# Kernel tuning notes

Hardware: AMD Instinct MI355X
Metric: run time of the kernel (lower is better)

Reference implementation:

```python
import jax, jax.numpy as jnp
import numpy as np

NEG_INF = jnp.float32(-1e30)


def setup_inputs() -> dict:
    key = jax.random.key(0)
    k1, k2, k3, k4 = jax.random.split(key, 4)
    B, L1, L2, H = 64, 1024, 1024, 128
    x = jax.random.normal(k1, (B, L1, H), dtype=jnp.float32)
    y = jax.random.normal(k2, (B, L2, H), dtype=jnp.float32)
    y_mask = jax.random.uniform(k3, (B, L2)) < 0.2
    W = jax.random.normal(k4, (H, H), dtype=jnp.float32) * (1.0 / np.sqrt(H))
    b = jnp.zeros((H,), dtype=jnp.float32)
    return {"x": x, "y": y, "y_mask": y_mask, "W": W, "b": b}


def reference(x, y, y_mask, W, b):
    # shared linear + relu projections (torch Linear: x @ W.T + b)
    x_proj = jax.nn.relu(jnp.einsum("bld,hd->blh", x, W) + b)  # [B, L1, H]
    y_proj = jax.nn.relu(jnp.einsum("bld,hd->blh", y, W) + b)  # [B, L2, H]
    # unscaled cross-attention scores
    scores = jnp.einsum("bih,bjh->bij", x_proj, y_proj)  # [B, L1, L2]
    scores = jnp.where(y_mask[:, None, :], NEG_INF, scores)
    alpha = jax.nn.softmax(scores, axis=-1)  # [B, L1, L2]
    # weighted sum over original (unprojected) y
    matched_seq = jnp.einsum("bij,bjh->bih", alpha, y)  # [B, L1, H]
    return matched_seq
```

## Files before the change

kernel.cpp:

```cpp
#include <hip/hip_runtime.h>
#include <hip/hip_bf16.h>


typedef __attribute__((ext_vector_type(8))) short    s8v;
typedef __attribute__((ext_vector_type(8))) _Float16 h8v;
typedef __attribute__((ext_vector_type(4))) float    f4v;

#define BDIM 256

__device__ __forceinline__ f4v mfma_bf16(s8v a, s8v b, f4v c) {
    return __builtin_amdgcn_mfma_f32_16x16x32_bf16(a, b, c, 0, 0, 0);
}
__device__ __forceinline__ f4v mfma_f16(h8v a, h8v b, f4v c) {
    return __builtin_amdgcn_mfma_f32_16x16x32_f16(a, b, c, 0, 0, 0);
}
__device__ __forceinline__ void tsplit(float v, short& hi, short& lo) {
    unsigned b = __builtin_bit_cast(unsigned, v);
    unsigned hb = b & 0xFFFF0000u;
    float res = v - __builtin_bit_cast(float, hb);
    hi = (short)(hb >> 16);
    lo = (short)(__builtin_bit_cast(unsigned, res) >> 16);
}

typedef const __attribute__((address_space(1))) unsigned int gu32;
typedef __attribute__((address_space(3))) unsigned int lu32;
__device__ __forceinline__ void gld_lds16(const void* g, void* l) {
    __builtin_amdgcn_global_load_lds((gu32*)g, (lu32*)l, 16, 0, 0);
}

__global__ __launch_bounds__(1024) void prep_kernel(
    const unsigned int* __restrict__ mraw, unsigned char* __restrict__ nm,
    const float* __restrict__ W, short* __restrict__ Whsw, short* __restrict__ Wlsw,
    const float* __restrict__ Y, _Float16* __restrict__ YTsw)
{
    if (blockIdx.x >= 2) {
        const int tb = blockIdx.x - 2;
        const int b = tb >> 4, jt = tb & 15;
        __shared__ _Float16 sT[128][64];
        const int tid = threadIdx.x;
        const int h = tid & 127, c0 = tid >> 7;
        const float* yb = Y + (size_t)(b * 1024 + jt * 64 + c0 * 8) * 128 + h;
        h8v hv;
        for (int k = 0; k < 8; ++k) hv[k] = (_Float16)yb[k * 128];
        *(h8v*)&sT[h][(c0 ^ (h & 7)) << 3] = hv;
        __syncthreads();
        *(h8v*)(YTsw + (size_t)tb * 8192 + tid * 8) =
            *(const h8v*)(&sT[0][0] + tid * 8);
        return;
    }
    if (blockIdx.x == 1) {
        for (int idx = threadIdx.x; idx < 16384; idx += 1024) {
            int r = idx >> 7, c = idx & 127;
            short hi, lo; tsplit(W[idx], hi, lo);
            int cs = (((c >> 3) ^ (r & 15)) << 3) | (c & 7);
            Whsw[r * 128 + cs] = hi;
            Wlsw[r * 128 + cs] = lo;
        }
        return;
    }
    __shared__ unsigned int sOrAll, sOrOdd;
    if (threadIdx.x == 0) { sOrAll = 0u; sOrOdd = 0u; }
    __syncthreads();
    unsigned int oa = 0u, oo = 0u;
    for (int i = threadIdx.x; i < 16384; i += 1024) {
        unsigned int v = mraw[i];
        oa |= v;
        if (i & 1) oo |= v;
    }
    atomicOr(&sOrAll, oa);
    atomicOr(&sOrOdd, oo);
    __syncthreads();
    const unsigned int orv = sOrAll, oro = sOrOdd;
    int mode;
    if (orv <= 1u)                       mode = (orv == 1u && oro == 0u) ? 3 : 0;
    else if ((orv & 0xFEFEFEFEu) == 0u)  mode = 1;
    else if ((orv & 0x0000FFFFu) == 0u)  mode = 0;
    else                                 mode = 2;
    const unsigned char*  b8  = (const unsigned char*)mraw;
    const unsigned short* b16 = (const unsigned short*)mraw;
    for (int j = threadIdx.x; j < 65536; j += 1024) {
        unsigned int v;
        if (mode == 0)      v = mraw[j];
        else if (mode == 1) v = b8[j];
        else if (mode == 2) v = b16[j];
        else                v = mraw[2 * j] | mraw[2 * j + 1];
        nm[j] = v ? 1 : 0;
    }
}

__global__ __launch_bounds__(BDIM, 4) void proj_kernel(
    const float* __restrict__ X, const float* __restrict__ Y,
    const short* __restrict__ Whsw, const short* __restrict__ Wlsw,
    const float* __restrict__ bias,
    _Float16* __restrict__ XPf, _Float16* __restrict__ YPsw)
{
    __shared__ short sW[2][64][128];

    const int gid = blockIdx.x;
    const float* src; int local;
    if (gid < 1024) { src = X; local = gid; }
    else            { src = Y; local = gid - 1024; }
    const int row0 = (local >> 1) * 128, h0 = (local & 1) * 64;
    const int t = threadIdx.x, w = t >> 6, lane = t & 63, c = lane & 15, q = lane >> 4;

    {
        const short* g0 = Whsw + h0 * 128;
        const short* g1 = Wlsw + h0 * 128;
        short* l0 = &sW[0][0][0];
        short* l1 = &sW[1][0][0];
        for (int i = 0; i < 4; ++i) {
            int off = (t + i * BDIM) * 8;
            *(s8v*)(l0 + off) = *(const s8v*)(g0 + off);
            *(s8v*)(l1 + off) = *(const s8v*)(g1 + off);
        }
    }

    f4v rawA[2][4], rawB[2][4];
#pragma unroll
    for (int set = 0; set < 2; ++set) {
        const float* xr = src + (size_t)(row0 + w * 32 + set * 16 + c) * 128;
#pragma unroll
        for (int ks = 0; ks < 4; ++ks) {
            rawA[set][ks] = *(const f4v*)&xr[ks * 32 + q * 8];
            rawB[set][ks] = *(const f4v*)&xr[ks * 32 + q * 8 + 4];
        }
    }
    __syncthreads();

    f4v zero = {0.f, 0.f, 0.f, 0.f};
#pragma unroll
    for (int set = 0; set < 2; ++set) {
        s8v ah[4], al[4];
#pragma unroll
        for (int ks = 0; ks < 4; ++ks) {
            for (int k = 0; k < 4; ++k) {
                short hh, ll;
                tsplit(rawA[set][ks][k], hh, ll); ah[ks][k] = hh;     al[ks][k] = ll;
                tsplit(rawB[set][ks][k], hh, ll); ah[ks][4 + k] = hh; al[ks][4 + k] = ll;
            }
        }
        f4v acc[4];
        for (int n = 0; n < 4; ++n) acc[n] = zero;
#pragma unroll
        for (int ks = 0; ks < 4; ++ks) {
            s8v bh[4], bl[4];
            for (int nt = 0; nt < 4; ++nt) {
                int cs = (((ks * 4 + q) ^ c) << 3);
                bh[nt] = *(const s8v*)&sW[0][nt * 16 + c][cs];
                bl[nt] = *(const s8v*)&sW[1][nt * 16 + c][cs];
            }
            for (int nt = 0; nt < 4; ++nt) {
                acc[nt] = mfma_bf16(ah[ks], bh[nt], acc[nt]);
                acc[nt] = mfma_bf16(al[ks], bh[nt], acc[nt]);
                acc[nt] = mfma_bf16(ah[ks], bl[nt], acc[nt]);
            }
        }
        for (int nt = 0; nt < 4; ++nt) {
            float bv = bias[h0 + nt * 16 + c];
            for (int r = 0; r < 4; ++r) {
                float v = fmaxf(acc[nt][r] + bv, 0.0f);
                int grow = row0 + w * 32 + set * 16 + q * 4 + r;
                int h = h0 + nt * 16 + c;
                if (gid < 1024) {
                    XPf[(size_t)grow * 128 + h] = (_Float16)v;
                } else {
                    int jt = (grow >> 6) & 15, jr = grow & 63;
                    int chunk = (h >> 3) ^ (jr & 7);
                    size_t off = (size_t)((grow >> 10) * 16 + jt) * 8192
                                 + jr * 128 + chunk * 8 + (h & 7);
                    YPsw[off] = (_Float16)v;
                }
            }
        }
    }
}

__global__ __launch_bounds__(BDIM, 2) void attn_kernel(
    const _Float16* __restrict__ YPsw, const _Float16* __restrict__ YTsw,
    const unsigned char* __restrict__ nmask,
    const _Float16* __restrict__ XPf, float* __restrict__ out)
{
    __shared__ _Float16 sTile[2][16384];
    __shared__ _Float16 sP[64][72];

    const int id = blockIdx.x;
    const int xcd = id & 7, rest = id >> 3;
    const int ibase = (rest & 15) * 64;
    const int b = xcd + 8 * (rest >> 4);
    const int t = threadIdx.x, wave = t >> 6, lane = t & 63;
    const int c = lane & 15, q = lane >> 4;
    const int mrow = b * 1024;

    h8v afrag[4];
    {
        const _Float16* xr = XPf + (size_t)(mrow + ibase + wave * 16 + c) * 128;
        for (int ks = 0; ks < 4; ++ks)
            afrag[ks] = *(const h8v*)&xr[ks * 32 + q * 8];
    }

    const char* gYP = (const char*)(YPsw + (size_t)b * 16 * 8192);
    const char* gYT = (const char*)(YTsw + (size_t)b * 16 * 8192);
    const int soff = wave * 1024 + lane * 16;

    {
        const char* gp = gYP + soff;
        const char* gt = gYT + soff;
        char* lp = (char*)&sTile[0][0]    + wave * 1024;
        char* lt = (char*)&sTile[0][8192] + wave * 1024;
        for (int i = 0; i < 4; ++i) {
            gld_lds16(gp + i * 4096, lp + i * 4096);
            gld_lds16(gt + i * 4096, lt + i * 4096);
        }
    }

    unsigned mw[4];
    for (int nt = 0; nt < 4; ++nt)
        mw[nt] = *(const unsigned*)(nmask + mrow + nt * 16 + q * 4);

    f4v zero = {0.f, 0.f, 0.f, 0.f};
    float m_s = -INFINITY, l_s = 0.f;
    f4v o[8];
    for (int h = 0; h < 8; ++h) o[h] = zero;

    const int srcbase = (lane & 48) + ((lane >> 4) << 2);
    const int cb = q ^ (c & 7);

    __syncthreads();

    int cur = 0;
    for (int jt = 0; jt < 16; ++jt) {
        const int jbase = jt * 64;
        const int nx = cur ^ 1;

        if (jt < 15) {
            const char* gp = gYP + (size_t)(jt + 1) * 16384 + soff;
            const char* gt = gYT + (size_t)(jt + 1) * 16384 + soff;
            char* lp = (char*)&sTile[nx][0]    + wave * 1024;
            char* lt = (char*)&sTile[nx][8192] + wave * 1024;
            for (int i = 0; i < 4; ++i) {
                gld_lds16(gp + i * 4096, lp + i * 4096);
                gld_lds16(gt + i * 4096, lt + i * 4096);
            }
        }

        f4v s[4];
        __builtin_amdgcn_s_setprio(1);
        for (int nt = 0; nt < 4; ++nt) {
            const _Float16* rp = &sTile[cur][0] + (nt * 16 + c) * 128;
            h8v f0 = *(const h8v*)(rp + ((cb ^ 0) << 3));
            h8v f1 = *(const h8v*)(rp + ((cb ^ 4) << 3));
            h8v f2 = *(const h8v*)(rp + ((cb ^ 8) << 3));
            h8v f3 = *(const h8v*)(rp + ((cb ^ 12) << 3));
            f4v acc = zero;
            acc = mfma_f16(f0, afrag[0], acc);
            acc = mfma_f16(f1, afrag[1], acc);
            acc = mfma_f16(f2, afrag[2], acc);
            acc = mfma_f16(f3, afrag[3], acc);
            s[nt] = acc;
        }
        __builtin_amdgcn_s_setprio(0);

        for (int nt = 0; nt < 4; ++nt)
            for (int r = 0; r < 4; ++r)
                if ((mw[nt] >> (r * 8)) & 0xFFu) s[nt][r] = -1e30f;

        float mx = fmaxf(
            fmaxf(fmaxf(fmaxf(s[0][0], s[0][1]), fmaxf(s[0][2], s[0][3])),
                  fmaxf(fmaxf(s[1][0], s[1][1]), fmaxf(s[1][2], s[1][3]))),
            fmaxf(fmaxf(fmaxf(s[2][0], s[2][1]), fmaxf(s[2][2], s[2][3])),
                  fmaxf(fmaxf(s[3][0], s[3][1]), fmaxf(s[3][2], s[3][3]))));
        mx = fmaxf(mx, __shfl_xor(mx, 16, 64));
        mx = fmaxf(mx, __shfl_xor(mx, 32, 64));
        float mnew = fmaxf(m_s, mx);
        float alpha = __expf(m_s - mnew);
        m_s = mnew;

        float rsum = 0.f;
        for (int nt = 0; nt < 4; ++nt)
            for (int r = 0; r < 4; ++r) {
                float p = ((mw[nt] >> (r * 8)) & 0xFFu) ? 0.f
                          : __expf(s[nt][r] - mnew);
                _Float16 ph = (_Float16)p;
                rsum += (float)ph;
                sP[wave * 16 + c][nt * 16 + q * 4 + r] = ph;
            }
        rsum += __shfl_xor(rsum, 16, 64);
        rsum += __shfl_xor(rsum, 32, 64);
        l_s = l_s * alpha + rsum;

        if (jt < 15) {
            const int jn = jbase + 64;
            for (int nt = 0; nt < 4; ++nt)
                mw[nt] = *(const unsigned*)(nmask + mrow + jn + nt * 16 + q * 4);
        }

        float aD0 = __shfl(alpha, srcbase + 0, 64);
        float aD1 = __shfl(alpha, srcbase + 1, 64);
        float aD2 = __shfl(alpha, srcbase + 2, 64);
        float aD3 = __shfl(alpha, srcbase + 3, 64);
        for (int h = 0; h < 8; ++h) {
            o[h][0] *= aD0; o[h][1] *= aD1; o[h][2] *= aD2; o[h][3] *= aD3;
        }

        __builtin_amdgcn_s_setprio(1);
        for (int k2 = 0; k2 < 2; ++k2) {
            h8v a = *(const h8v*)&sP[wave * 16 + c][k2 * 32 + q * 8];
            const _Float16* yt = &sTile[cur][8192];
            for (int hb = 0; hb < 8; ++hb) {
                h8v bb = *(const h8v*)(yt + (hb * 16 + c) * 64
                                       + ((((k2 << 2) + q) ^ (c & 7)) << 3));
                o[hb] = mfma_f16(a, bb, o[hb]);
            }
        }
        __builtin_amdgcn_s_setprio(0);

        __syncthreads();
        cur = nx;
    }

    float lD[4];
    lD[0] = __shfl(l_s, srcbase + 0, 64);
    lD[1] = __shfl(l_s, srcbase + 1, 64);
    lD[2] = __shfl(l_s, srcbase + 2, 64);
    lD[3] = __shfl(l_s, srcbase + 3, 64);
    for (int h = 0; h < 8; ++h) {
        for (int r = 0; r < 4; ++r) {
            float v = o[h][r] / lD[r];
            out[(size_t)(mrow + ibase + wave * 16 + q * 4 + r) * 128 + h * 16 + c] = v;
        }
    }
}

extern "C" void kernel_launch(void* const* d_in, const int* in_sizes, int n_in,
                              void* d_out, int out_size, void* d_ws, size_t ws_size,
                              hipStream_t stream) {
    const float* x    = (const float*)d_in[0];
    const float* y    = (const float*)d_in[1];
    const unsigned int* mraw = (const unsigned int*)d_in[2];
    const float* W    = (const float*)d_in[3];
    const float* bias = (const float*)d_in[4];
    float* out = (float*)d_out;

    unsigned char* nmask = (unsigned char*)d_ws;
    short* Whsw = (short*)((char*)d_ws + 65536);
    short* Wlsw = Whsw + 16384;
    _Float16* XPf = (_Float16*)(Wlsw + 16384);
    _Float16* YPsw = XPf + (size_t)64 * 1024 * 128;
    _Float16* YTsw = YPsw + (size_t)64 * 1024 * 128;

    prep_kernel<<<1026, 1024, 0, stream>>>(mraw, nmask, W, Whsw, Wlsw, y, YTsw);
    proj_kernel<<<2048, BDIM, 0, stream>>>(x, y, Whsw, Wlsw, bias, XPf, YPsw);
    attn_kernel<<<1024, BDIM, 0, stream>>>(YPsw, YTsw, nmask, XPf, out);
}
```

Measured before the change: 227.7 us.

## Double attention block to 128 query rows and swizzle P tile in LDS

Each attention block now handles 128 query rows with 8 waves (512 threads) instead of 64 rows with 4 waves. The shared Y tiles are therefore reused by twice as many rows, which halves the global-to-LDS traffic per query row, and each thread issues half as many async loads. The P staging buffer is rewritten with XOR-swizzled 4-wide vector stores, replacing scalar padded stores, to reduce LDS bank conflicts and store count. The trade-off is fewer blocks in the grid (512), which may lower occupancy and latency hiding, plus more LDS use per block.

```diff
diff --git a/kernel.cpp b/kernel.cpp
--- a/kernel.cpp
+++ b/kernel.cpp
@@ -4,6 +4,7 @@
 
 typedef __attribute__((ext_vector_type(8))) short    s8v;
 typedef __attribute__((ext_vector_type(8))) _Float16 h8v;
+typedef __attribute__((ext_vector_type(4))) _Float16 h4v;
 typedef __attribute__((ext_vector_type(4))) float    f4v;
 
 #define BDIM 256
@@ -175,18 +176,18 @@
     }
 }
 
-__global__ __launch_bounds__(BDIM, 2) void attn_kernel(
+__global__ __launch_bounds__(512, 4) void attn_kernel(
     const _Float16* __restrict__ YPsw, const _Float16* __restrict__ YTsw,
     const unsigned char* __restrict__ nmask,
     const _Float16* __restrict__ XPf, float* __restrict__ out)
 {
     __shared__ _Float16 sTile[2][16384];
-    __shared__ _Float16 sP[64][72];
+    __shared__ _Float16 sP[128 * 64];
 
     const int id = blockIdx.x;
     const int xcd = id & 7, rest = id >> 3;
-    const int ibase = (rest & 15) * 64;
-    const int b = xcd + 8 * (rest >> 4);
+    const int ibase = (rest & 7) * 128;
+    const int b = xcd + 8 * (rest >> 3);
     const int t = threadIdx.x, wave = t >> 6, lane = t & 63;
     const int c = lane & 15, q = lane >> 4;
     const int mrow = b * 1024;
@@ -203,13 +204,11 @@
     const int soff = wave * 1024 + lane * 16;
 
     {
-        const char* gp = gYP + soff;
-        const char* gt = gYT + soff;
         char* lp = (char*)&sTile[0][0]    + wave * 1024;
         char* lt = (char*)&sTile[0][8192] + wave * 1024;
-        for (int i = 0; i < 4; ++i) {
-            gld_lds16(gp + i * 4096, lp + i * 4096);
-            gld_lds16(gt + i * 4096, lt + i * 4096);
+        for (int i = 0; i < 2; ++i) {
+            gld_lds16(gYP + soff + i * 8192, lp + i * 8192);
+            gld_lds16(gYT + soff + i * 8192, lt + i * 8192);
         }
     }
 
@@ -224,6 +223,8 @@
 
     const int srcbase = (lane & 48) + ((lane >> 4) << 2);
     const int cb = q ^ (c & 7);
+    const int prow = (wave * 16 + c) * 64;
+    const int pwofs = (q & 1) * 4;
 
     __syncthreads();
 
@@ -233,13 +234,13 @@
         const int nx = cur ^ 1;
 
         if (jt < 15) {
-            const char* gp = gYP + (size_t)(jt + 1) * 16384 + soff;
-            const char* gt = gYT + (size_t)(jt + 1) * 16384 + soff;
+            const char* gp = gYP + (size_t)(jt + 1) * 16384;
+            const char* gt = gYT + (size_t)(jt + 1) * 16384;
             char* lp = (char*)&sTile[nx][0]    + wave * 1024;
             char* lt = (char*)&sTile[nx][8192] + wave * 1024;
-            for (int i = 0; i < 4; ++i) {
-                gld_lds16(gp + i * 4096, lp + i * 4096);
-                gld_lds16(gt + i * 4096, lt + i * 4096);
+            for (int i = 0; i < 2; ++i) {
+                gld_lds16(gp + soff + i * 8192, lp + i * 8192);
+                gld_lds16(gt + soff + i * 8192, lt + i * 8192);
             }
         }
 
@@ -276,14 +277,18 @@
         m_s = mnew;
 
         float rsum = 0.f;
-        for (int nt = 0; nt < 4; ++nt)
+        for (int nt = 0; nt < 4; ++nt) {
+            h4v ph4;
             for (int r = 0; r < 4; ++r) {
                 float p = ((mw[nt] >> (r * 8)) & 0xFFu) ? 0.f
                           : __expf(s[nt][r] - mnew);
                 _Float16 ph = (_Float16)p;
                 rsum += (float)ph;
-                sP[wave * 16 + c][nt * 16 + q * 4 + r] = ph;
-            }
+                ph4[r] = ph;
+            }
+            int ck = (2 * nt + (q >> 1)) ^ (c & 7);
+            *(h4v*)&sP[prow + ck * 8 + pwofs] = ph4;
+        }
         rsum += __shfl_xor(rsum, 16, 64);
         rsum += __shfl_xor(rsum, 32, 64);
         l_s = l_s * alpha + rsum;
@@ -304,7 +309,7 @@
 
         __builtin_amdgcn_s_setprio(1);
         for (int k2 = 0; k2 < 2; ++k2) {
-            h8v a = *(const h8v*)&sP[wave * 16 + c][k2 * 32 + q * 8];
+            h8v a = *(const h8v*)&sP[prow + (((k2 << 2) + q) ^ (c & 7)) * 8];
             const _Float16* yt = &sTile[cur][8192];
             for (int hb = 0; hb < 8; ++hb) {
                 h8v bb = *(const h8v*)(yt + (hb * 16 + c) * 64
@@ -350,5 +355,5 @@
 
     prep_kernel<<<1026, 1024, 0, stream>>>(mraw, nmask, W, Whsw, Wlsw, y, YTsw);
     proj_kernel<<<2048, BDIM, 0, stream>>>(x, y, Whsw, Wlsw, bias, XPf, YPsw);
-    attn_kernel<<<1024, BDIM, 0, stream>>>(YPsw, YTsw, nmask, XPf, out);
-}
+    attn_kernel<<<512, 512, 0, stream>>>(YPsw, YTsw, nmask, XPf, out);
+}
```

After: 215.0 us. -5.6%, faster.
